# Kernel tuning notes

Hardware: AMD Instinct MI355X
Metric: run time of the kernel (lower is better)

The kernel has to match this reference:

```python
import jax, jax.numpy as jnp
import numpy as np

NUM_EXPERTS = 8
TOP_K = 2
HIDDEN = 512
INTER = 2048
BALANCE_COEF = 0.01


def setup_inputs() -> dict:
    key = jax.random.key(0)
    ks = jax.random.split(key, 5)
    B, S = 2, 1024
    scale_in = 1.0 / np.sqrt(HIDDEN)
    scale_mid = 1.0 / np.sqrt(INTER)
    return {
        "hidden_states": jax.random.normal(ks[0], (B, S, HIDDEN), jnp.float32),
        "w_router": jax.random.normal(ks[1], (HIDDEN, NUM_EXPERTS), jnp.float32) * scale_in,
        "b_router": jnp.zeros((NUM_EXPERTS,), jnp.float32),
        "w1": jax.random.normal(ks[2], (NUM_EXPERTS, HIDDEN, INTER), jnp.float32) * scale_in,
        "b1": jnp.zeros((NUM_EXPERTS, INTER), jnp.float32),
        "w2": jax.random.normal(ks[3], (NUM_EXPERTS, INTER, HIDDEN), jnp.float32) * scale_mid,
        "b2": jnp.zeros((NUM_EXPERTS, HIDDEN), jnp.float32),
    }


def reference(hidden_states, w_router, b_router, w1, b1, w2, b2):
    B, S, H = hidden_states.shape
    E, K = NUM_EXPERTS, TOP_K

    # ---- Router: softmax over experts, top-k selection, renormalized weights ----
    logits = jnp.einsum("bsh,he->bse", hidden_states, w_router) + b_router  # (B,S,E)
    probs = jax.nn.softmax(logits, axis=-1)
    top_vals, top_idx = jax.lax.top_k(probs, K)                              # (B,S,K)
    routing_weights = top_vals / jnp.sum(top_vals, axis=-1, keepdims=True)   # renorm to sum 1

    # ---- Load-balancing auxiliary loss: coef * E * sum_e f_e * P_e ----
    assign = jax.nn.one_hot(top_idx, E, dtype=probs.dtype)                   # (B,S,K,E)
    f = jnp.mean(assign, axis=(0, 1, 2))                                     # fraction routed per expert
    P = jnp.mean(probs, axis=(0, 1))                                         # mean router prob per expert
    balance_loss = BALANCE_COEF * E * jnp.sum(f * P)

    # ---- Phase 1: flatten (B,S,H) -> (B*S*K, H) token-slots ----
    T = B * S * K
    tokens_flat = jnp.broadcast_to(hidden_states[:, :, None, :], (B, S, K, H)).reshape(T, H)
    weights_flat = routing_weights.reshape(T)
    experts_flat = top_idx.reshape(T)

    # ---- Phase 2: per-expert MLP, masked combine ----
    out_flat = jnp.zeros_like(tokens_flat)
    for e in range(E):
        hmid = jax.nn.gelu(tokens_flat @ w1[e] + b1[e])                      # (T, INTER)
        y = hmid @ w2[e] + b2[e]                                             # (T, H)
        mask = (experts_flat == e)
        out_flat = out_flat + jnp.where(mask[:, None], y * weights_flat[:, None], 0.0)

    # ---- Phase 3: combine over K and residual ----
    combined = out_flat.reshape(B, S, K, H).sum(axis=2)
    output = combined + hidden_states
    return output, balance_loss
```

## Files before the change

kernel.cpp:

```cpp
#include <hip/hip_runtime.h>
#include <math.h>

#define NT 2048
#define TSLOTS 4096
#define HID 512
#define INTER 2048
#define NE 8
#define TM 128
#define BKG 64
#define MAXTILES 40
#define PSLOTS 5120
#define KZ2 4

#define WS_HMID      0
#define WS_PROBS     0
#define WS_TOPIDX    65536
#define WS_TOPW      81920
#define WS_TILE_E    20971520
#define WS_TILE_B    20972032
#define WS_TILE_V    20972544
#define WS_PERM      20973056
#define WS_PW        20993536
#define WS_ISLOT     21014016
#define WS_XB        21030400
#define WS_W1T       23127552
#define WS_W2T       39904768
#define WS_Y         56681984

typedef __attribute__((ext_vector_type(8))) short bf16x8;
typedef __attribute__((ext_vector_type(4))) float f32x4;
typedef __attribute__((ext_vector_type(8))) unsigned short ushort8;

__device__ __forceinline__ unsigned short f2bf(float f) {
    union { float f; unsigned u; } v; v.f = f;
    unsigned r = v.u + 0x7FFF + ((v.u >> 16) & 1);
    return (unsigned short)(r >> 16);
}
__device__ __forceinline__ float bf2f(unsigned short b) {
    union { unsigned u; float f; } v; v.u = ((unsigned)b) << 16;
    return v.f;
}

__device__ __forceinline__ void gload16(const void* g, void* l) {
    __builtin_amdgcn_global_load_lds(
        (const __attribute__((address_space(1))) unsigned int*)g,
        (__attribute__((address_space(3))) unsigned int*)l, 16, 0, 0);
}

__device__ __forceinline__ float gelu_fast(float x) {
    float t = 1.5957691f * x + 0.0713548f * x * x * x;
    return x / (1.0f + __expf(-t));
}

__global__ __launch_bounds__(256) void route_k(
    const float* __restrict__ hs, const float* __restrict__ wr,
    const float* __restrict__ br,
    unsigned short* __restrict__ xb,
    float* __restrict__ probs, int* __restrict__ topidx, float* __restrict__ topw)
{
    int tid = threadIdx.x;
    int lane = tid & 63, wave = tid >> 6;
    int t = blockIdx.x * 4 + wave;
    const float* x = hs + (size_t)t * HID + lane * 8;
    float4 v0 = *(const float4*)x;
    float4 v1 = *(const float4*)(x + 4);

    ushort8 ob;
    ob[0] = f2bf(v0.x); ob[1] = f2bf(v0.y); ob[2] = f2bf(v0.z); ob[3] = f2bf(v0.w);
    ob[4] = f2bf(v1.x); ob[5] = f2bf(v1.y); ob[6] = f2bf(v1.z); ob[7] = f2bf(v1.w);
    *(ushort8*)(xb + (size_t)t * HID + lane * 8) = ob;

    float xv[8] = {v0.x, v0.y, v0.z, v0.w, v1.x, v1.y, v1.z, v1.w};
    float acc[NE];
#pragma unroll
    for (int e = 0; e < NE; e++) acc[e] = 0.0f;
    const float* w = wr + (size_t)lane * 8 * NE;
#pragma unroll
    for (int j = 0; j < 8; j++) {
        float4 wa = *(const float4*)(w + j * NE);
        float4 wb = *(const float4*)(w + j * NE + 4);
        acc[0] += xv[j] * wa.x; acc[1] += xv[j] * wa.y;
        acc[2] += xv[j] * wa.z; acc[3] += xv[j] * wa.w;
        acc[4] += xv[j] * wb.x; acc[5] += xv[j] * wb.y;
        acc[6] += xv[j] * wb.z; acc[7] += xv[j] * wb.w;
    }
#pragma unroll
    for (int off = 32; off > 0; off >>= 1) {
#pragma unroll
        for (int e = 0; e < NE; e++) acc[e] += __shfl_down(acc[e], off);
    }
    if (lane == 0) {
        float l[NE], p[NE];
        float m = -1e30f;
#pragma unroll
        for (int e = 0; e < NE; e++) { l[e] = acc[e] + br[e]; m = fmaxf(m, l[e]); }
        float s = 0.0f;
#pragma unroll
        for (int e = 0; e < NE; e++) { p[e] = expf(l[e] - m); s += p[e]; }
        float inv = 1.0f / s;
#pragma unroll
        for (int e = 0; e < NE; e++) { p[e] *= inv; probs[(size_t)t * NE + e] = p[e]; }
        int i1 = 0;
#pragma unroll
        for (int e = 1; e < NE; e++) if (p[e] > p[i1]) i1 = e;
        int i2 = (i1 == 0) ? 1 : 0;
#pragma unroll
        for (int e = 0; e < NE; e++) if (e != i1 && p[e] > p[i2]) i2 = e;
        float denom = 1.0f / (p[i1] + p[i2]);
        topidx[2 * t]     = i1;
        topidx[2 * t + 1] = i2;
        topw[2 * t]       = p[i1] * denom;
        topw[2 * t + 1]   = p[i2] * denom;
    }
}

__global__ __launch_bounds__(256) void tp_k(
    const float* __restrict__ w1, const float* __restrict__ w2,
    unsigned short* __restrict__ w1t, unsigned short* __restrict__ w2t,
    const float* __restrict__ probs, const int* __restrict__ topidx,
    const float* __restrict__ topw,
    int* __restrict__ tile_e, int* __restrict__ tile_b, int* __restrict__ tile_v,
    int* __restrict__ perm, float* __restrict__ pw, int* __restrict__ islot,
    float* __restrict__ loss_out)
{
    int tid = threadIdx.x;
    if (blockIdx.x == 0) {
        int lane = tid & 63, wave = tid >> 6;
        float ps[NE];
        int c[NE];
#pragma unroll
        for (int e = 0; e < NE; e++) { ps[e] = 0.0f; c[e] = 0; }
        for (int t = tid; t < NT; t += 256) {
            float4 p0 = *(const float4*)&probs[(size_t)t * NE];
            float4 p1 = *(const float4*)&probs[(size_t)t * NE + 4];
            ps[0] += p0.x; ps[1] += p0.y; ps[2] += p0.z; ps[3] += p0.w;
            ps[4] += p1.x; ps[5] += p1.y; ps[6] += p1.z; ps[7] += p1.w;
        }
        for (int t = tid; t < TSLOTS; t += 256) c[topidx[t]]++;
#pragma unroll
        for (int off = 32; off > 0; off >>= 1) {
#pragma unroll
            for (int e = 0; e < NE; e++) {
                ps[e] += __shfl_down(ps[e], off);
                c[e]  += __shfl_down(c[e], off);
            }
        }
        __shared__ float sps[4][NE];
        __shared__ int sc[4][NE];
        __shared__ int scur[NE], sbase[NE], scnt[NE], spref[NE + 1];
        if (lane == 0) {
#pragma unroll
            for (int e = 0; e < NE; e++) { sps[wave][e] = ps[e]; sc[wave][e] = c[e]; }
        }
        __syncthreads();
        if (tid == 0) {
            float loss = 0.0f;
            int b = 0, tp = 0;
            for (int e = 0; e < NE; e++) {
                float pse = sps[0][e] + sps[1][e] + sps[2][e] + sps[3][e];
                int ce = sc[0][e] + sc[1][e] + sc[2][e] + sc[3][e];
                loss += ((float)ce / (float)TSLOTS) * (pse / (float)NT);
                int nt = (ce + TM - 1) / TM;
                sbase[e] = b; scnt[e] = ce; scur[e] = b; spref[e] = tp;
                tp += nt;
                b += nt * TM;
            }
            spref[NE] = tp;
            loss_out[0] = 0.01f * (float)NE * loss;
        }
        __syncthreads();
        for (int tx = tid; tx < MAXTILES; tx += 256) {
            if (tx >= spref[NE]) { tile_e[tx] = -1; continue; }
            int e = 0;
            while (tx >= spref[e + 1]) e++;
            int i = tx - spref[e];
            tile_e[tx] = e;
            tile_b[tx] = sbase[e] + i * TM;
            int v = scnt[e] - i * TM;
            tile_v[tx] = v > TM ? TM : v;
        }
        __syncthreads();
        for (int t = tid; t < TSLOTS; t += 256) {
            int e = topidx[t];
            int p = atomicAdd(&scur[e], 1);
            perm[p] = t;
            pw[p] = topw[t];
            islot[t] = p;
        }
        return;
    }

    __shared__ float T[32][33];
    int t = blockIdx.x - 1;
    const float* src;
    unsigned short* dst;
    int K, N, n0, k0;
    if (t < 8192) {
        int e = t >> 10, rem = t & 1023;
        n0 = (rem & 63) * 32; k0 = (rem >> 6) * 32;
        src = w1 + (size_t)e * HID * INTER;
        dst = w1t + (size_t)e * INTER * HID;
        K = HID; N = INTER;
    } else {
        t -= 8192;
        int e = t >> 10, rem = t & 1023;
        n0 = (rem & 15) * 32; k0 = (rem >> 4) * 32;
        src = w2 + (size_t)e * INTER * HID;
        dst = w2t + (size_t)e * HID * INTER;
        K = INTER; N = HID;
    }
    int r = tid >> 3, c4 = (tid & 7) * 4;
    float4 v = *(const float4*)(src + (size_t)(k0 + r) * N + n0 + c4);
    T[r][c4 + 0] = v.x; T[r][c4 + 1] = v.y; T[r][c4 + 2] = v.z; T[r][c4 + 3] = v.w;
    __syncthreads();
    ushort4 o;
    o.x = f2bf(T[c4 + 0][r]); o.y = f2bf(T[c4 + 1][r]);
    o.z = f2bf(T[c4 + 2][r]); o.w = f2bf(T[c4 + 3][r]);
    *(ushort4*)(dst + (size_t)(n0 + r) * K + k0 + c4) = o;
}

__global__ __launch_bounds__(256) void gemm1_k(
    const unsigned short* __restrict__ xb, const unsigned short* __restrict__ w1t,
    const float* __restrict__ b1,
    const int* __restrict__ tile_e, const int* __restrict__ tile_b,
    const int* __restrict__ tile_v, const int* __restrict__ perm,
    unsigned short* __restrict__ hmid)
{
    int tt = blockIdx.y;
    int e = tile_e[tt];
    if (e < 0) return;
    int p0 = tile_b[tt], nv = tile_v[tt];
    int n0 = blockIdx.x * 128;

    __shared__ unsigned short As[128 * 64];
    __shared__ unsigned short Bs[128 * 64];

    int tid = threadIdx.x;
    int lane = tid & 63, wave = tid >> 6;
    int wm = (wave >> 1) * 64, wn = (wave & 1) * 64;

    int rb = tid >> 3;
    int g = (tid & 7) ^ (rb & 7);
    const unsigned short* ap[4];
    const unsigned short* bp[4];
    const unsigned short* bbase = w1t + (size_t)e * INTER * HID;
#pragma unroll
    for (int i = 0; i < 4; i++) {
        int r = rb + i * 32;
        int tok = perm[p0 + ((r < nv) ? r : 0)] >> 1;
        ap[i] = xb + (size_t)tok * HID + g * 8;
        bp[i] = bbase + (size_t)(n0 + r) * HID + g * 8;
    }

    f32x4 acc[4][4] = {};
    int fm = lane & 15, fq = lane >> 4;

    for (int k0 = 0; k0 < HID; k0 += BKG) {
        __syncthreads();
#pragma unroll
        for (int i = 0; i < 4; i++) gload16(ap[i] + k0, (void*)(As + (tid + i * 256) * 8));
#pragma unroll
        for (int i = 0; i < 4; i++) gload16(bp[i] + k0, (void*)(Bs + (tid + i * 256) * 8));
        __syncthreads();
#pragma unroll
        for (int kk = 0; kk < 2; kk++) {
            bf16x8 af[4], bfr[4];
#pragma unroll
            for (int mt = 0; mt < 4; mt++) {
                int R = wm + mt * 16 + fm;
                int G = (kk * 4 + fq) ^ (R & 7);
                af[mt] = *(const bf16x8*)&As[R * 64 + G * 8];
            }
#pragma unroll
            for (int nt = 0; nt < 4; nt++) {
                int R = wn + nt * 16 + fm;
                int G = (kk * 4 + fq) ^ (R & 7);
                bfr[nt] = *(const bf16x8*)&Bs[R * 64 + G * 8];
            }
#pragma unroll
            for (int mt = 0; mt < 4; mt++)
#pragma unroll
                for (int nt = 0; nt < 4; nt++)
                    acc[mt][nt] = __builtin_amdgcn_mfma_f32_16x16x32_bf16(
                        bfr[nt], af[mt], acc[mt][nt], 0, 0, 0);
        }
    }

    int cm = lane & 15, qn = (lane >> 4) * 4;
#pragma unroll
    for (int mt = 0; mt < 4; mt++) {
        int m = wm + mt * 16 + cm;
        size_t rowoff = (size_t)(p0 + m) * INTER;
#pragma unroll
        for (int nt = 0; nt < 4; nt++) {
            int nb = n0 + wn + nt * 16 + qn;
            float4 bb = *(const float4*)(b1 + e * INTER + nb);
            ushort4 o;
            o.x = f2bf(gelu_fast(acc[mt][nt][0] + bb.x));
            o.y = f2bf(gelu_fast(acc[mt][nt][1] + bb.y));
            o.z = f2bf(gelu_fast(acc[mt][nt][2] + bb.z));
            o.w = f2bf(gelu_fast(acc[mt][nt][3] + bb.w));
            *(ushort4*)(hmid + rowoff + nb) = o;
        }
    }
}

__global__ __launch_bounds__(256) void gemm2_k(
    const unsigned short* __restrict__ hmid, const unsigned short* __restrict__ w2t,
    const float* __restrict__ b2,
    const int* __restrict__ tile_e, const int* __restrict__ tile_b,
    unsigned short* __restrict__ y)
{
    int tt = blockIdx.y;
    int e = tile_e[tt];
    if (e < 0) return;
    int p0 = tile_b[tt];
    int n0 = blockIdx.x * 128;
    int kz = blockIdx.z;
    int kbeg = kz * (INTER / KZ2), kend = kbeg + INTER / KZ2;
    unsigned short* yk = y + (size_t)kz * PSLOTS * HID;

    __shared__ unsigned short As[128 * 64];
    __shared__ unsigned short Bs[128 * 64];

    int tid = threadIdx.x;
    int lane = tid & 63, wave = tid >> 6;
    int wm = (wave >> 1) * 64, wn = (wave & 1) * 64;

    int rb = tid >> 3;
    int g = (tid & 7) ^ (rb & 7);
    const unsigned short* ap[4];
    const unsigned short* bp[4];
    const unsigned short* bbase = w2t + (size_t)e * HID * INTER;
#pragma unroll
    for (int i = 0; i < 4; i++) {
        int r = rb + i * 32;
        ap[i] = hmid + (size_t)(p0 + r) * INTER + g * 8;
        bp[i] = bbase + (size_t)(n0 + r) * INTER + g * 8;
    }

    f32x4 acc[4][4] = {};
    int fm = lane & 15, fq = lane >> 4;

    for (int k0 = kbeg; k0 < kend; k0 += BKG) {
        __syncthreads();
#pragma unroll
        for (int i = 0; i < 4; i++) gload16(ap[i] + k0, (void*)(As + (tid + i * 256) * 8));
#pragma unroll
        for (int i = 0; i < 4; i++) gload16(bp[i] + k0, (void*)(Bs + (tid + i * 256) * 8));
        __syncthreads();
#pragma unroll
        for (int kk = 0; kk < 2; kk++) {
            bf16x8 af[4], bfr[4];
#pragma unroll
            for (int mt = 0; mt < 4; mt++) {
                int R = wm + mt * 16 + fm;
                int G = (kk * 4 + fq) ^ (R & 7);
                af[mt] = *(const bf16x8*)&As[R * 64 + G * 8];
            }
#pragma unroll
            for (int nt = 0; nt < 4; nt++) {
                int R = wn + nt * 16 + fm;
                int G = (kk * 4 + fq) ^ (R & 7);
                bfr[nt] = *(const bf16x8*)&Bs[R * 64 + G * 8];
            }
#pragma unroll
            for (int mt = 0; mt < 4; mt++)
#pragma unroll
                for (int nt = 0; nt < 4; nt++)
                    acc[mt][nt] = __builtin_amdgcn_mfma_f32_16x16x32_bf16(
                        bfr[nt], af[mt], acc[mt][nt], 0, 0, 0);
        }
    }

    int cm = lane & 15, qn = (lane >> 4) * 4;
#pragma unroll
    for (int mt = 0; mt < 4; mt++) {
        int m = wm + mt * 16 + cm;
        size_t rowoff = (size_t)(p0 + m) * HID;
#pragma unroll
        for (int nt = 0; nt < 4; nt++) {
            int nb = n0 + wn + nt * 16 + qn;
            float4 bb = (kz == 0) ? *(const float4*)(b2 + e * HID + nb)
                                  : float4{0.0f, 0.0f, 0.0f, 0.0f};
            ushort4 o;
            o.x = f2bf(acc[mt][nt][0] + bb.x);
            o.y = f2bf(acc[mt][nt][1] + bb.y);
            o.z = f2bf(acc[mt][nt][2] + bb.z);
            o.w = f2bf(acc[mt][nt][3] + bb.w);
            *(ushort4*)(yk + rowoff + nb) = o;
        }
    }
}

__global__ __launch_bounds__(256) void combine_k(
    const float* __restrict__ hs, const unsigned short* __restrict__ y,
    const int* __restrict__ islot, const float* __restrict__ pw,
    float* __restrict__ out)
{
    int tid = threadIdx.x;
    int lane = tid & 63, wave = tid >> 6;
    int t = blockIdx.x * 4 + wave;
    int pA = islot[2 * t], pB = islot[2 * t + 1];
    float wA = pw[pA], wB = pw[pB];
    int c = lane * 8;
    float oa[8] = {}, ob[8] = {};
#pragma unroll
    for (int z = 0; z < KZ2; z++) {
        ushort8 a = *(const ushort8*)(y + (size_t)z * PSLOTS * HID + (size_t)pA * HID + c);
        ushort8 b = *(const ushort8*)(y + (size_t)z * PSLOTS * HID + (size_t)pB * HID + c);
#pragma unroll
        for (int j = 0; j < 8; j++) { oa[j] += bf2f(a[j]); ob[j] += bf2f(b[j]); }
    }
    const float* h = hs + (size_t)t * HID + c;
    float4 h0 = *(const float4*)h;
    float4 h1 = *(const float4*)(h + 4);
    float4 r0 = {wA * oa[0] + wB * ob[0] + h0.x, wA * oa[1] + wB * ob[1] + h0.y,
                 wA * oa[2] + wB * ob[2] + h0.z, wA * oa[3] + wB * ob[3] + h0.w};
    float4 r1 = {wA * oa[4] + wB * ob[4] + h1.x, wA * oa[5] + wB * ob[5] + h1.y,
                 wA * oa[6] + wB * ob[6] + h1.z, wA * oa[7] + wB * ob[7] + h1.w};
    float* op = out + (size_t)t * HID + c;
    *(float4*)op = r0;
    *(float4*)(op + 4) = r1;
}

extern "C" void kernel_launch(void* const* d_in, const int* in_sizes, int n_in,
                              void* d_out, int out_size, void* d_ws, size_t ws_size,
                              hipStream_t stream) {
    const float* hs = (const float*)d_in[0];
    const float* wr = (const float*)d_in[1];
    const float* br = (const float*)d_in[2];
    const float* w1 = (const float*)d_in[3];
    const float* b1 = (const float*)d_in[4];
    const float* w2 = (const float*)d_in[5];
    const float* b2 = (const float*)d_in[6];
    float* out = (float*)d_out;

    char* ws = (char*)d_ws;
    float* probs           = (float*)(ws + WS_PROBS);
    int*   topidx          = (int*)(ws + WS_TOPIDX);
    float* topw            = (float*)(ws + WS_TOPW);
    int*   tile_e          = (int*)(ws + WS_TILE_E);
    int*   tile_b          = (int*)(ws + WS_TILE_B);
    int*   tile_v          = (int*)(ws + WS_TILE_V);
    int*   perm            = (int*)(ws + WS_PERM);
    float* pw              = (float*)(ws + WS_PW);
    int*   islot           = (int*)(ws + WS_ISLOT);
    unsigned short* xb     = (unsigned short*)(ws + WS_XB);
    unsigned short* w1t    = (unsigned short*)(ws + WS_W1T);
    unsigned short* w2t    = (unsigned short*)(ws + WS_W2T);
    unsigned short* hmid   = (unsigned short*)(ws + WS_HMID);
    unsigned short* y      = (unsigned short*)(ws + WS_Y);

    route_k<<<NT / 4, 256, 0, stream>>>(hs, wr, br, xb, probs, topidx, topw);
    tp_k<<<1 + 16384, 256, 0, stream>>>(w1, w2, w1t, w2t, probs, topidx, topw,
                                        tile_e, tile_b, tile_v, perm, pw, islot,
                                        out + (size_t)NT * HID);
    gemm1_k<<<dim3(INTER / 128, MAXTILES), 256, 0, stream>>>(
        xb, w1t, b1, tile_e, tile_b, tile_v, perm, hmid);
    gemm2_k<<<dim3(HID / 128, MAXTILES, KZ2), 256, 0, stream>>>(
        hmid, w2t, b2, tile_e, tile_b, y);
    combine_k<<<NT / 4, 256, 0, stream>>>(hs, y, islot, pw, out);
}
```

Baseline: 190.8 us.

## Fuse all MoE stages into one persistent cooperative kernel with grid syncs

Replaces the five separate launches (routing, weight transpose/dispatch, two grouped GEMMs, combine) with a single cooperative persistent kernel that loops over work items and uses grid-wide syncs between phases. It also halves the split-K factor for the second GEMM. The aim is to cut launch overhead and inter-kernel gaps. In exchange, grid barriers add cost, the grid is capped by occupancy, and the smaller split-K leaves less parallelism in GEMM2.

```diff
diff --git a/kernel.cpp b/kernel.cpp
--- a/kernel.cpp
+++ b/kernel.cpp
@@ -1,5 +1,8 @@
 #include <hip/hip_runtime.h>
+#include <hip/hip_cooperative_groups.h>
 #include <math.h>
+
+namespace cg = cooperative_groups;
 
 #define NT 2048
 #define TSLOTS 4096
@@ -10,7 +13,7 @@
 #define BKG 64
 #define MAXTILES 40
 #define PSLOTS 5120
-#define KZ2 4
+#define KZ2 2
 
 #define WS_HMID      0
 #define WS_PROBS     0
@@ -40,92 +43,108 @@
     union { unsigned u; float f; } v; v.u = ((unsigned)b) << 16;
     return v.f;
 }
-
 __device__ __forceinline__ void gload16(const void* g, void* l) {
     __builtin_amdgcn_global_load_lds(
         (const __attribute__((address_space(1))) unsigned int*)g,
         (__attribute__((address_space(3))) unsigned int*)l, 16, 0, 0);
 }
-
 __device__ __forceinline__ float gelu_fast(float x) {
     float t = 1.5957691f * x + 0.0713548f * x * x * x;
     return x / (1.0f + __expf(-t));
 }
 
-__global__ __launch_bounds__(256) void route_k(
+__global__ __launch_bounds__(256) void moe_k(
     const float* __restrict__ hs, const float* __restrict__ wr,
-    const float* __restrict__ br,
-    unsigned short* __restrict__ xb,
-    float* __restrict__ probs, int* __restrict__ topidx, float* __restrict__ topw)
+    const float* __restrict__ br, const float* __restrict__ w1,
+    const float* __restrict__ b1, const float* __restrict__ w2,
+    const float* __restrict__ b2, float* __restrict__ out,
+    char* __restrict__ ws)
 {
+    cg::grid_group gg = cg::this_grid();
+    __shared__ __align__(16) unsigned char smem[32768];
+
+    float* probs         = (float*)(ws + WS_PROBS);
+    int* topidx          = (int*)(ws + WS_TOPIDX);
+    float* topw          = (float*)(ws + WS_TOPW);
+    int* tile_e          = (int*)(ws + WS_TILE_E);
+    int* tile_b          = (int*)(ws + WS_TILE_B);
+    int* tile_v          = (int*)(ws + WS_TILE_V);
+    int* perm            = (int*)(ws + WS_PERM);
+    float* pw            = (float*)(ws + WS_PW);
+    int* islot           = (int*)(ws + WS_ISLOT);
+    unsigned short* xb   = (unsigned short*)(ws + WS_XB);
+    unsigned short* w1t  = (unsigned short*)(ws + WS_W1T);
+    unsigned short* w2t  = (unsigned short*)(ws + WS_W2T);
+    unsigned short* hmid = (unsigned short*)(ws + WS_HMID);
+    unsigned short* y    = (unsigned short*)(ws + WS_Y);
+    float* loss_out      = out + (size_t)NT * HID;
+
     int tid = threadIdx.x;
     int lane = tid & 63, wave = tid >> 6;
-    int t = blockIdx.x * 4 + wave;
-    const float* x = hs + (size_t)t * HID + lane * 8;
-    float4 v0 = *(const float4*)x;
-    float4 v1 = *(const float4*)(x + 4);
-
-    ushort8 ob;
-    ob[0] = f2bf(v0.x); ob[1] = f2bf(v0.y); ob[2] = f2bf(v0.z); ob[3] = f2bf(v0.w);
-    ob[4] = f2bf(v1.x); ob[5] = f2bf(v1.y); ob[6] = f2bf(v1.z); ob[7] = f2bf(v1.w);
-    *(ushort8*)(xb + (size_t)t * HID + lane * 8) = ob;
-
-    float xv[8] = {v0.x, v0.y, v0.z, v0.w, v1.x, v1.y, v1.z, v1.w};
-    float acc[NE];
-#pragma unroll
-    for (int e = 0; e < NE; e++) acc[e] = 0.0f;
-    const float* w = wr + (size_t)lane * 8 * NE;
-#pragma unroll
-    for (int j = 0; j < 8; j++) {
-        float4 wa = *(const float4*)(w + j * NE);
-        float4 wb = *(const float4*)(w + j * NE + 4);
-        acc[0] += xv[j] * wa.x; acc[1] += xv[j] * wa.y;
-        acc[2] += xv[j] * wa.z; acc[3] += xv[j] * wa.w;
-        acc[4] += xv[j] * wb.x; acc[5] += xv[j] * wb.y;
-        acc[6] += xv[j] * wb.z; acc[7] += xv[j] * wb.w;
+    int nb = gridDim.x;
+
+    for (int j = blockIdx.x; j < NT / 4; j += nb) {
+        int t = j * 4 + wave;
+        const float* x = hs + (size_t)t * HID + lane * 8;
+        float4 v0 = *(const float4*)x;
+        float4 v1 = *(const float4*)(x + 4);
+        ushort8 ob;
+        ob[0] = f2bf(v0.x); ob[1] = f2bf(v0.y); ob[2] = f2bf(v0.z); ob[3] = f2bf(v0.w);
+        ob[4] = f2bf(v1.x); ob[5] = f2bf(v1.y); ob[6] = f2bf(v1.z); ob[7] = f2bf(v1.w);
+        *(ushort8*)(xb + (size_t)t * HID + lane * 8) = ob;
+
+        float xv[8] = {v0.x, v0.y, v0.z, v0.w, v1.x, v1.y, v1.z, v1.w};
+        float acc[NE];
+#pragma unroll
+        for (int e = 0; e < NE; e++) acc[e] = 0.0f;
+        const float* w = wr + (size_t)lane * 8 * NE;
+#pragma unroll
+        for (int jj = 0; jj < 8; jj++) {
+            float4 wa = *(const float4*)(w + jj * NE);
+            float4 wb = *(const float4*)(w + jj * NE + 4);
+            acc[0] += xv[jj] * wa.x; acc[1] += xv[jj] * wa.y;
+            acc[2] += xv[jj] * wa.z; acc[3] += xv[jj] * wa.w;
+            acc[4] += xv[jj] * wb.x; acc[5] += xv[jj] * wb.y;
+            acc[6] += xv[jj] * wb.z; acc[7] += xv[jj] * wb.w;
+        }
+#pragma unroll
+        for (int off = 32; off > 0; off >>= 1) {
+#pragma unroll
+            for (int e = 0; e < NE; e++) acc[e] += __shfl_down(acc[e], off);
+        }
+        if (lane == 0) {
+            float l[NE], p[NE];
+            float m = -1e30f;
+#pragma unroll
+            for (int e = 0; e < NE; e++) { l[e] = acc[e] + br[e]; m = fmaxf(m, l[e]); }
+            float s = 0.0f;
+#pragma unroll
+            for (int e = 0; e < NE; e++) { p[e] = expf(l[e] - m); s += p[e]; }
+            float inv = 1.0f / s;
+#pragma unroll
+            for (int e = 0; e < NE; e++) { p[e] *= inv; probs[(size_t)t * NE + e] = p[e]; }
+            int i1 = 0;
+#pragma unroll
+            for (int e = 1; e < NE; e++) if (p[e] > p[i1]) i1 = e;
+            int i2 = (i1 == 0) ? 1 : 0;
+#pragma unroll
+            for (int e = 0; e < NE; e++) if (e != i1 && p[e] > p[i2]) i2 = e;
+            float denom = 1.0f / (p[i1] + p[i2]);
+            topidx[2 * t]     = i1;
+            topidx[2 * t + 1] = i2;
+            topw[2 * t]       = p[i1] * denom;
+            topw[2 * t + 1]   = p[i2] * denom;
+        }
     }
-#pragma unroll
-    for (int off = 32; off > 0; off >>= 1) {
-#pragma unroll
-        for (int e = 0; e < NE; e++) acc[e] += __shfl_down(acc[e], off);
-    }
-    if (lane == 0) {
-        float l[NE], p[NE];
-        float m = -1e30f;
-#pragma unroll
-        for (int e = 0; e < NE; e++) { l[e] = acc[e] + br[e]; m = fmaxf(m, l[e]); }
-        float s = 0.0f;
-#pragma unroll
-        for (int e = 0; e < NE; e++) { p[e] = expf(l[e] - m); s += p[e]; }
-        float inv = 1.0f / s;
-#pragma unroll
-        for (int e = 0; e < NE; e++) { p[e] *= inv; probs[(size_t)t * NE + e] = p[e]; }
-        int i1 = 0;
-#pragma unroll
-        for (int e = 1; e < NE; e++) if (p[e] > p[i1]) i1 = e;
-        int i2 = (i1 == 0) ? 1 : 0;
-#pragma unroll
-        for (int e = 0; e < NE; e++) if (e != i1 && p[e] > p[i2]) i2 = e;
-        float denom = 1.0f / (p[i1] + p[i2]);
-        topidx[2 * t]     = i1;
-        topidx[2 * t + 1] = i2;
-        topw[2 * t]       = p[i1] * denom;
-        topw[2 * t + 1]   = p[i2] * denom;
-    }
-}
-
-__global__ __launch_bounds__(256) void tp_k(
-    const float* __restrict__ w1, const float* __restrict__ w2,
-    unsigned short* __restrict__ w1t, unsigned short* __restrict__ w2t,
-    const float* __restrict__ probs, const int* __restrict__ topidx,
-    const float* __restrict__ topw,
-    int* __restrict__ tile_e, int* __restrict__ tile_b, int* __restrict__ tile_v,
-    int* __restrict__ perm, float* __restrict__ pw, int* __restrict__ islot,
-    float* __restrict__ loss_out)
-{
-    int tid = threadIdx.x;
+    gg.sync();
+
     if (blockIdx.x == 0) {
-        int lane = tid & 63, wave = tid >> 6;
+        float* sps = (float*)smem;
+        int* sc    = (int*)(smem + 128);
+        int* scur  = (int*)(smem + 256);
+        int* sbase = (int*)(smem + 288);
+        int* scnt  = (int*)(smem + 320);
+        int* spref = (int*)(smem + 352);
         float ps[NE];
         int c[NE];
 #pragma unroll
@@ -145,20 +164,17 @@
                 c[e]  += __shfl_down(c[e], off);
             }
         }
-        __shared__ float sps[4][NE];
-        __shared__ int sc[4][NE];
-        __shared__ int scur[NE], sbase[NE], scnt[NE], spref[NE + 1];
         if (lane == 0) {
 #pragma unroll
-            for (int e = 0; e < NE; e++) { sps[wave][e] = ps[e]; sc[wave][e] = c[e]; }
+            for (int e = 0; e < NE; e++) { sps[wave * NE + e] = ps[e]; sc[wave * NE + e] = c[e]; }
         }
         __syncthreads();
         if (tid == 0) {
             float loss = 0.0f;
             int b = 0, tp = 0;
             for (int e = 0; e < NE; e++) {
-                float pse = sps[0][e] + sps[1][e] + sps[2][e] + sps[3][e];
-                int ce = sc[0][e] + sc[1][e] + sc[2][e] + sc[3][e];
+                float pse = sps[e] + sps[NE + e] + sps[2 * NE + e] + sps[3 * NE + e];
+                int ce = sc[e] + sc[NE + e] + sc[2 * NE + e] + sc[3 * NE + e];
                 loss += ((float)ce / (float)TSLOTS) * (pse / (float)NT);
                 int nt = (ce + TM - 1) / TM;
                 sbase[e] = b; scnt[e] = ce; scur[e] = b; spref[e] = tp;
@@ -187,241 +203,210 @@
             pw[p] = topw[t];
             islot[t] = p;
         }
-        return;
+    } else {
+        float (*T)[33] = (float(*)[33])smem;
+        int r = tid >> 3, c4 = (tid & 7) * 4;
+        for (int t0 = blockIdx.x - 1; t0 < 16384; t0 += nb - 1) {
+            int t = t0;
+            const float* src;
+            unsigned short* dst;
+            int K, N, n0, k0;
+            if (t < 8192) {
+                int e = t >> 10, rem = t & 1023;
+                n0 = (rem & 63) * 32; k0 = (rem >> 6) * 32;
+                src = w1 + (size_t)e * HID * INTER;
+                dst = w1t + (size_t)e * INTER * HID;
+                K = HID; N = INTER;
+            } else {
+                t -= 8192;
+                int e = t >> 10, rem = t & 1023;
+                n0 = (rem & 15) * 32; k0 = (rem >> 4) * 32;
+                src = w2 + (size_t)e * INTER * HID;
+                dst = w2t + (size_t)e * HID * INTER;
+                K = INTER; N = HID;
+            }
+            float4 v = *(const float4*)(src + (size_t)(k0 + r) * N + n0 + c4);
+            T[r][c4 + 0] = v.x; T[r][c4 + 1] = v.y; T[r][c4 + 2] = v.z; T[r][c4 + 3] = v.w;
+            __syncthreads();
+            ushort4 o;
+            o.x = f2bf(T[c4 + 0][r]); o.y = f2bf(T[c4 + 1][r]);
+            o.z = f2bf(T[c4 + 2][r]); o.w = f2bf(T[c4 + 3][r]);
+            *(ushort4*)(dst + (size_t)(n0 + r) * K + k0 + c4) = o;
+            __syncthreads();
+        }
     }
-
-    __shared__ float T[32][33];
-    int t = blockIdx.x - 1;
-    const float* src;
-    unsigned short* dst;
-    int K, N, n0, k0;
-    if (t < 8192) {
-        int e = t >> 10, rem = t & 1023;
-        n0 = (rem & 63) * 32; k0 = (rem >> 6) * 32;
-        src = w1 + (size_t)e * HID * INTER;
-        dst = w1t + (size_t)e * INTER * HID;
-        K = HID; N = INTER;
-    } else {
-        t -= 8192;
-        int e = t >> 10, rem = t & 1023;
-        n0 = (rem & 15) * 32; k0 = (rem >> 4) * 32;
-        src = w2 + (size_t)e * INTER * HID;
-        dst = w2t + (size_t)e * HID * INTER;
-        K = INTER; N = HID;
-    }
-    int r = tid >> 3, c4 = (tid & 7) * 4;
-    float4 v = *(const float4*)(src + (size_t)(k0 + r) * N + n0 + c4);
-    T[r][c4 + 0] = v.x; T[r][c4 + 1] = v.y; T[r][c4 + 2] = v.z; T[r][c4 + 3] = v.w;
-    __syncthreads();
-    ushort4 o;
-    o.x = f2bf(T[c4 + 0][r]); o.y = f2bf(T[c4 + 1][r]);
-    o.z = f2bf(T[c4 + 2][r]); o.w = f2bf(T[c4 + 3][r]);
-    *(ushort4*)(dst + (size_t)(n0 + r) * K + k0 + c4) = o;
-}
-
-__global__ __launch_bounds__(256) void gemm1_k(
-    const unsigned short* __restrict__ xb, const unsigned short* __restrict__ w1t,
-    const float* __restrict__ b1,
-    const int* __restrict__ tile_e, const int* __restrict__ tile_b,
-    const int* __restrict__ tile_v, const int* __restrict__ perm,
-    unsigned short* __restrict__ hmid)
-{
-    int tt = blockIdx.y;
-    int e = tile_e[tt];
-    if (e < 0) return;
-    int p0 = tile_b[tt], nv = tile_v[tt];
-    int n0 = blockIdx.x * 128;
-
-    __shared__ unsigned short As[128 * 64];
-    __shared__ unsigned short Bs[128 * 64];
-
-    int tid = threadIdx.x;
-    int lane = tid & 63, wave = tid >> 6;
+    gg.sync();
+
+    unsigned short* As = (unsigned short*)smem;
+    unsigned short* Bs = (unsigned short*)(smem + 16384);
     int wm = (wave >> 1) * 64, wn = (wave & 1) * 64;
-
     int rb = tid >> 3;
     int g = (tid & 7) ^ (rb & 7);
-    const unsigned short* ap[4];
-    const unsigned short* bp[4];
-    const unsigned short* bbase = w1t + (size_t)e * INTER * HID;
-#pragma unroll
-    for (int i = 0; i < 4; i++) {
-        int r = rb + i * 32;
-        int tok = perm[p0 + ((r < nv) ? r : 0)] >> 1;
-        ap[i] = xb + (size_t)tok * HID + g * 8;
-        bp[i] = bbase + (size_t)(n0 + r) * HID + g * 8;
+    int fm = lane & 15, fq = lane >> 4;
+    int cm = lane & 15, qn = (lane >> 4) * 4;
+
+    for (int j = blockIdx.x; j < (INTER / 128) * MAXTILES; j += nb) {
+        int tt = j % MAXTILES, nblk = j / MAXTILES;
+        int e = tile_e[tt];
+        if (e < 0) continue;
+        int p0 = tile_b[tt], nv = tile_v[tt];
+        int n0 = nblk * 128;
+
+        const unsigned short* ap[4];
+        const unsigned short* bp[4];
+        const unsigned short* bbase = w1t + (size_t)e * INTER * HID;
+#pragma unroll
+        for (int i = 0; i < 4; i++) {
+            int r = rb + i * 32;
+            int tok = perm[p0 + ((r < nv) ? r : 0)] >> 1;
+            ap[i] = xb + (size_t)tok * HID + g * 8;
+            bp[i] = bbase + (size_t)(n0 + r) * HID + g * 8;
+        }
+        f32x4 acc[4][4] = {};
+        for (int k0 = 0; k0 < HID; k0 += BKG) {
+            __syncthreads();
+#pragma unroll
+            for (int i = 0; i < 4; i++) gload16(ap[i] + k0, (void*)(As + (tid + i * 256) * 8));
+#pragma unroll
+            for (int i = 0; i < 4; i++) gload16(bp[i] + k0, (void*)(Bs + (tid + i * 256) * 8));
+            __syncthreads();
+#pragma unroll
+            for (int kk = 0; kk < 2; kk++) {
+                bf16x8 af[4], bfr[4];
+#pragma unroll
+                for (int mt = 0; mt < 4; mt++) {
+                    int R = wm + mt * 16 + fm;
+                    int G = (kk * 4 + fq) ^ (R & 7);
+                    af[mt] = *(const bf16x8*)&As[R * 64 + G * 8];
+                }
+#pragma unroll
+                for (int nt = 0; nt < 4; nt++) {
+                    int R = wn + nt * 16 + fm;
+                    int G = (kk * 4 + fq) ^ (R & 7);
+                    bfr[nt] = *(const bf16x8*)&Bs[R * 64 + G * 8];
+                }
+#pragma unroll
+                for (int mt = 0; mt < 4; mt++)
+#pragma unroll
+                    for (int nt = 0; nt < 4; nt++)
+                        acc[mt][nt] = __builtin_amdgcn_mfma_f32_16x16x32_bf16(
+                            bfr[nt], af[mt], acc[mt][nt], 0, 0, 0);
+            }
+        }
+#pragma unroll
+        for (int mt = 0; mt < 4; mt++) {
+            int m = wm + mt * 16 + cm;
+            size_t rowoff = (size_t)(p0 + m) * INTER;
+#pragma unroll
+            for (int nt = 0; nt < 4; nt++) {
+                int nbv = n0 + wn + nt * 16 + qn;
+                float4 bb = *(const float4*)(b1 + e * INTER + nbv);
+                ushort4 o;
+                o.x = f2bf(gelu_fast(acc[mt][nt][0] + bb.x));
+                o.y = f2bf(gelu_fast(acc[mt][nt][1] + bb.y));
+                o.z = f2bf(gelu_fast(acc[mt][nt][2] + bb.z));
+                o.w = f2bf(gelu_fast(acc[mt][nt][3] + bb.w));
+                *(ushort4*)(hmid + rowoff + nbv) = o;
+            }
+        }
     }
-
-    f32x4 acc[4][4] = {};
-    int fm = lane & 15, fq = lane >> 4;
-
-    for (int k0 = 0; k0 < HID; k0 += BKG) {
-        __syncthreads();
-#pragma unroll
-        for (int i = 0; i < 4; i++) gload16(ap[i] + k0, (void*)(As + (tid + i * 256) * 8));
-#pragma unroll
-        for (int i = 0; i < 4; i++) gload16(bp[i] + k0, (void*)(Bs + (tid + i * 256) * 8));
-        __syncthreads();
-#pragma unroll
-        for (int kk = 0; kk < 2; kk++) {
-            bf16x8 af[4], bfr[4];
-#pragma unroll
-            for (int mt = 0; mt < 4; mt++) {
-                int R = wm + mt * 16 + fm;
-                int G = (kk * 4 + fq) ^ (R & 7);
-                af[mt] = *(const bf16x8*)&As[R * 64 + G * 8];
-            }
+    gg.sync();
+
+    for (int j = blockIdx.x; j < (HID / 128) * MAXTILES * KZ2; j += nb) {
+        int tt = j % MAXTILES;
+        int rem = j / MAXTILES;
+        int nblk = rem % (HID / 128), kz = rem / (HID / 128);
+        int e = tile_e[tt];
+        if (e < 0) continue;
+        int p0 = tile_b[tt];
+        int n0 = nblk * 128;
+        int kbeg = kz * (INTER / KZ2), kend = kbeg + INTER / KZ2;
+        unsigned short* yk = y + (size_t)kz * PSLOTS * HID;
+
+        const unsigned short* ap[4];
+        const unsigned short* bp[4];
+        const unsigned short* bbase = w2t + (size_t)e * HID * INTER;
+#pragma unroll
+        for (int i = 0; i < 4; i++) {
+            int r = rb + i * 32;
+            ap[i] = hmid + (size_t)(p0 + r) * INTER + g * 8;
+            bp[i] = bbase + (size_t)(n0 + r) * INTER + g * 8;
+        }
+        f32x4 acc[4][4] = {};
+        for (int k0 = kbeg; k0 < kend; k0 += BKG) {
+            __syncthreads();
+#pragma unroll
+            for (int i = 0; i < 4; i++) gload16(ap[i] + k0, (void*)(As + (tid + i * 256) * 8));
+#pragma unroll
+            for (int i = 0; i < 4; i++) gload16(bp[i] + k0, (void*)(Bs + (tid + i * 256) * 8));
+            __syncthreads();
+#pragma unroll
+            for (int kk = 0; kk < 2; kk++) {
+                bf16x8 af[4], bfr[4];
+#pragma unroll
+                for (int mt = 0; mt < 4; mt++) {
+                    int R = wm + mt * 16 + fm;
+                    int G = (kk * 4 + fq) ^ (R & 7);
+                    af[mt] = *(const bf16x8*)&As[R * 64 + G * 8];
+                }
+#pragma unroll
+                for (int nt = 0; nt < 4; nt++) {
+                    int R = wn + nt * 16 + fm;
+                    int G = (kk * 4 + fq) ^ (R & 7);
+                    bfr[nt] = *(const bf16x8*)&Bs[R * 64 + G * 8];
+                }
+#pragma unroll
+                for (int mt = 0; mt < 4; mt++)
+#pragma unroll
+                    for (int nt = 0; nt < 4; nt++)
+                        acc[mt][nt] = __builtin_amdgcn_mfma_f32_16x16x32_bf16(
+                            bfr[nt], af[mt], acc[mt][nt], 0, 0, 0);
+            }
+        }
+#pragma unroll
+        for (int mt = 0; mt < 4; mt++) {
+            int m = wm + mt * 16 + cm;
+            size_t rowoff = (size_t)(p0 + m) * HID;
 #pragma unroll
             for (int nt = 0; nt < 4; nt++) {
-                int R = wn + nt * 16 + fm;
-                int G = (kk * 4 + fq) ^ (R & 7);
-                bfr[nt] = *(const bf16x8*)&Bs[R * 64 + G * 8];
-            }
-#pragma unroll
-            for (int mt = 0; mt < 4; mt++)
-#pragma unroll
-                for (int nt = 0; nt < 4; nt++)
-                    acc[mt][nt] = __builtin_amdgcn_mfma_f32_16x16x32_bf16(
-                        bfr[nt], af[mt], acc[mt][nt], 0, 0, 0);
+                int nbv = n0 + wn + nt * 16 + qn;
+                float4 bb = (kz == 0) ? *(const float4*)(b2 + e * HID + nbv)
+                                      : float4{0.0f, 0.0f, 0.0f, 0.0f};
+                ushort4 o;
+                o.x = f2bf(acc[mt][nt][0] + bb.x);
+                o.y = f2bf(acc[mt][nt][1] + bb.y);
+                o.z = f2bf(acc[mt][nt][2] + bb.z);
+                o.w = f2bf(acc[mt][nt][3] + bb.w);
+                *(ushort4*)(yk + rowoff + nbv) = o;
+            }
         }
     }
-
-    int cm = lane & 15, qn = (lane >> 4) * 4;
-#pragma unroll
-    for (int mt = 0; mt < 4; mt++) {
-        int m = wm + mt * 16 + cm;
-        size_t rowoff = (size_t)(p0 + m) * INTER;
-#pragma unroll
-        for (int nt = 0; nt < 4; nt++) {
-            int nb = n0 + wn + nt * 16 + qn;
-            float4 bb = *(const float4*)(b1 + e * INTER + nb);
-            ushort4 o;
-            o.x = f2bf(gelu_fast(acc[mt][nt][0] + bb.x));
-            o.y = f2bf(gelu_fast(acc[mt][nt][1] + bb.y));
-            o.z = f2bf(gelu_fast(acc[mt][nt][2] + bb.z));
-            o.w = f2bf(gelu_fast(acc[mt][nt][3] + bb.w));
-            *(ushort4*)(hmid + rowoff + nb) = o;
-        }
+    gg.sync();
+
+    for (int j = blockIdx.x; j < NT / 4; j += nb) {
+        int t = j * 4 + wave;
+        int pA = islot[2 * t], pB = islot[2 * t + 1];
+        float wA = pw[pA], wB = pw[pB];
+        int c = lane * 8;
+        float oa[8] = {}, obv[8] = {};
+#pragma unroll
+        for (int z = 0; z < KZ2; z++) {
+            ushort8 a = *(const ushort8*)(y + (size_t)z * PSLOTS * HID + (size_t)pA * HID + c);
+            ushort8 b = *(const ushort8*)(y + (size_t)z * PSLOTS * HID + (size_t)pB * HID + c);
+#pragma unroll
+            for (int jj = 0; jj < 8; jj++) { oa[jj] += bf2f(a[jj]); obv[jj] += bf2f(b[jj]); }
+        }
+        const float* h = hs + (size_t)t * HID + c;
+        float4 h0 = *(const float4*)h;
+        float4 h1 = *(const float4*)(h + 4);
+        float4 r0 = {wA * oa[0] + wB * obv[0] + h0.x, wA * oa[1] + wB * obv[1] + h0.y,
+                     wA * oa[2] + wB * obv[2] + h0.z, wA * oa[3] + wB * obv[3] + h0.w};
+        float4 r1 = {wA * oa[4] + wB * obv[4] + h1.x, wA * oa[5] + wB * obv[5] + h1.y,
+                     wA * oa[6] + wB * obv[6] + h1.z, wA * oa[7] + wB * obv[7] + h1.w};
+        float* op = out + (size_t)t * HID + c;
+        *(float4*)op = r0;
+        *(float4*)(op + 4) = r1;
     }
-}
-
-__global__ __launch_bounds__(256) void gemm2_k(
-    const unsigned short* __restrict__ hmid, const unsigned short* __restrict__ w2t,
-    const float* __restrict__ b2,
-    const int* __restrict__ tile_e, const int* __restrict__ tile_b,
-    unsigned short* __restrict__ y)
-{
-    int tt = blockIdx.y;
-    int e = tile_e[tt];
-    if (e < 0) return;
-    int p0 = tile_b[tt];
-    int n0 = blockIdx.x * 128;
-    int kz = blockIdx.z;
-    int kbeg = kz * (INTER / KZ2), kend = kbeg + INTER / KZ2;
-    unsigned short* yk = y + (size_t)kz * PSLOTS * HID;
-
-    __shared__ unsigned short As[128 * 64];
-    __shared__ unsigned short Bs[128 * 64];
-
-    int tid = threadIdx.x;
-    int lane = tid & 63, wave = tid >> 6;
-    int wm = (wave >> 1) * 64, wn = (wave & 1) * 64;
-
-    int rb = tid >> 3;
-    int g = (tid & 7) ^ (rb & 7);
-    const unsigned short* ap[4];
-    const unsigned short* bp[4];
-    const unsigned short* bbase = w2t + (size_t)e * HID * INTER;
-#pragma unroll
-    for (int i = 0; i < 4; i++) {
-        int r = rb + i * 32;
-        ap[i] = hmid + (size_t)(p0 + r) * INTER + g * 8;
-        bp[i] = bbase + (size_t)(n0 + r) * INTER + g * 8;
-    }
-
-    f32x4 acc[4][4] = {};
-    int fm = lane & 15, fq = lane >> 4;
-
-    for (int k0 = kbeg; k0 < kend; k0 += BKG) {
-        __syncthreads();
-#pragma unroll
-        for (int i = 0; i < 4; i++) gload16(ap[i] + k0, (void*)(As + (tid + i * 256) * 8));
-#pragma unroll
-        for (int i = 0; i < 4; i++) gload16(bp[i] + k0, (void*)(Bs + (tid + i * 256) * 8));
-        __syncthreads();
-#pragma unroll
-        for (int kk = 0; kk < 2; kk++) {
-            bf16x8 af[4], bfr[4];
-#pragma unroll
-            for (int mt = 0; mt < 4; mt++) {
-                int R = wm + mt * 16 + fm;
-                int G = (kk * 4 + fq) ^ (R & 7);
-                af[mt] = *(const bf16x8*)&As[R * 64 + G * 8];
-            }
-#pragma unroll
-            for (int nt = 0; nt < 4; nt++) {
-                int R = wn + nt * 16 + fm;
-                int G = (kk * 4 + fq) ^ (R & 7);
-                bfr[nt] = *(const bf16x8*)&Bs[R * 64 + G * 8];
-            }
-#pragma unroll
-            for (int mt = 0; mt < 4; mt++)
-#pragma unroll
-                for (int nt = 0; nt < 4; nt++)
-                    acc[mt][nt] = __builtin_amdgcn_mfma_f32_16x16x32_bf16(
-                        bfr[nt], af[mt], acc[mt][nt], 0, 0, 0);
-        }
-    }
-
-    int cm = lane & 15, qn = (lane >> 4) * 4;
-#pragma unroll
-    for (int mt = 0; mt < 4; mt++) {
-        int m = wm + mt * 16 + cm;
-        size_t rowoff = (size_t)(p0 + m) * HID;
-#pragma unroll
-        for (int nt = 0; nt < 4; nt++) {
-            int nb = n0 + wn + nt * 16 + qn;
-            float4 bb = (kz == 0) ? *(const float4*)(b2 + e * HID + nb)
-                                  : float4{0.0f, 0.0f, 0.0f, 0.0f};
-            ushort4 o;
-            o.x = f2bf(acc[mt][nt][0] + bb.x);
-            o.y = f2bf(acc[mt][nt][1] + bb.y);
-            o.z = f2bf(acc[mt][nt][2] + bb.z);
-            o.w = f2bf(acc[mt][nt][3] + bb.w);
-            *(ushort4*)(yk + rowoff + nb) = o;
-        }
-    }
-}
-
-__global__ __launch_bounds__(256) void combine_k(
-    const float* __restrict__ hs, const unsigned short* __restrict__ y,
-    const int* __restrict__ islot, const float* __restrict__ pw,
-    float* __restrict__ out)
-{
-    int tid = threadIdx.x;
-    int lane = tid & 63, wave = tid >> 6;
-    int t = blockIdx.x * 4 + wave;
-    int pA = islot[2 * t], pB = islot[2 * t + 1];
-    float wA = pw[pA], wB = pw[pB];
-    int c = lane * 8;
-    float oa[8] = {}, ob[8] = {};
-#pragma unroll
-    for (int z = 0; z < KZ2; z++) {
-        ushort8 a = *(const ushort8*)(y + (size_t)z * PSLOTS * HID + (size_t)pA * HID + c);
-        ushort8 b = *(const ushort8*)(y + (size_t)z * PSLOTS * HID + (size_t)pB * HID + c);
-#pragma unroll
-        for (int j = 0; j < 8; j++) { oa[j] += bf2f(a[j]); ob[j] += bf2f(b[j]); }
-    }
-    const float* h = hs + (size_t)t * HID + c;
-    float4 h0 = *(const float4*)h;
-    float4 h1 = *(const float4*)(h + 4);
-    float4 r0 = {wA * oa[0] + wB * ob[0] + h0.x, wA * oa[1] + wB * ob[1] + h0.y,
-                 wA * oa[2] + wB * ob[2] + h0.z, wA * oa[3] + wB * ob[3] + h0.w};
-    float4 r1 = {wA * oa[4] + wB * ob[4] + h1.x, wA * oa[5] + wB * ob[5] + h1.y,
-                 wA * oa[6] + wB * ob[6] + h1.z, wA * oa[7] + wB * ob[7] + h1.w};
-    float* op = out + (size_t)t * HID + c;
-    *(float4*)op = r0;
-    *(float4*)(op + 4) = r1;
 }
 
 extern "C" void kernel_launch(void* const* d_in, const int* in_sizes, int n_in,
@@ -435,30 +420,16 @@
     const float* w2 = (const float*)d_in[5];
     const float* b2 = (const float*)d_in[6];
     float* out = (float*)d_out;
-
     char* ws = (char*)d_ws;
-    float* probs           = (float*)(ws + WS_PROBS);
-    int*   topidx          = (int*)(ws + WS_TOPIDX);
-    float* topw            = (float*)(ws + WS_TOPW);
-    int*   tile_e          = (int*)(ws + WS_TILE_E);
-    int*   tile_b          = (int*)(ws + WS_TILE_B);
-    int*   tile_v          = (int*)(ws + WS_TILE_V);
-    int*   perm            = (int*)(ws + WS_PERM);
-    float* pw              = (float*)(ws + WS_PW);
-    int*   islot           = (int*)(ws + WS_ISLOT);
-    unsigned short* xb     = (unsigned short*)(ws + WS_XB);
-    unsigned short* w1t    = (unsigned short*)(ws + WS_W1T);
-    unsigned short* w2t    = (unsigned short*)(ws + WS_W2T);
-    unsigned short* hmid   = (unsigned short*)(ws + WS_HMID);
-    unsigned short* y      = (unsigned short*)(ws + WS_Y);
-
-    route_k<<<NT / 4, 256, 0, stream>>>(hs, wr, br, xb, probs, topidx, topw);
-    tp_k<<<1 + 16384, 256, 0, stream>>>(w1, w2, w1t, w2t, probs, topidx, topw,
-                                        tile_e, tile_b, tile_v, perm, pw, islot,
-                                        out + (size_t)NT * HID);
-    gemm1_k<<<dim3(INTER / 128, MAXTILES), 256, 0, stream>>>(
-        xb, w1t, b1, tile_e, tile_b, tile_v, perm, hmid);
-    gemm2_k<<<dim3(HID / 128, MAXTILES, KZ2), 256, 0, stream>>>(
-        hmid, w2t, b2, tile_e, tile_b, y);
-    combine_k<<<NT / 4, 256, 0, stream>>>(hs, y, islot, pw, out);
-}
+
+    int nbpc = 0;
+    if (hipOccupancyMaxActiveBlocksPerMultiprocessor(&nbpc, moe_k, 256, 0) != hipSuccess
+        || nbpc < 1) nbpc = 1;
+    int grid = nbpc * 256;
+    if (grid < 2) grid = 2;
+
+    void* args[] = {(void*)&hs, (void*)&wr, (void*)&br, (void*)&w1, (void*)&b1,
+                    (void*)&w2, (void*)&b2, (void*)&out, (void*)&ws};
+    (void)hipLaunchCooperativeKernel((const void*)moe_k, dim3(grid), dim3(256),
+                                     args, 0, stream);
+}
```

Measured after the change: 375.5 us. +96.9%, slower.
